# Optimization experiments

Measured on AMD Instinct MI355X. Metric: run time of the kernel, lower is better.

Reference implementation:

```python
import jax, jax.numpy as jnp
import numpy as np

N, D, F = 4096, 4096, 16384  # tokens, d_model, d_ff


def setup_inputs() -> dict:
    key = jax.random.key(0)
    ks = jax.random.split(key, 8)
    q_in = jax.random.randint(ks[0], (N, D), -127, 128, dtype=jnp.int32)
    in_scale = jax.random.uniform(ks[1], (N,), dtype=jnp.float32) * 0.01 + 1e-4
    w1_q = jax.random.randint(ks[2], (F, D), -127, 128, dtype=jnp.int32)
    w1_scale = jax.random.uniform(ks[3], (F,), dtype=jnp.float32) * 0.01 + 1e-4
    b1 = jax.random.normal(ks[4], (F,), dtype=jnp.float32) * 0.02
    w2_q = jax.random.randint(ks[5], (D, F), -127, 128, dtype=jnp.int32)
    w2_scale = jax.random.uniform(ks[6], (D,), dtype=jnp.float32) * 0.01 + 1e-4
    b2 = jax.random.normal(ks[7], (D,), dtype=jnp.float32) * 0.02
    return {"q_in": q_in, "in_scale": in_scale, "w1_q": w1_q, "w1_scale": w1_scale,
            "b1": b1, "w2_q": w2_q, "w2_scale": w2_scale, "b2": b2}


def _dynamic_quant(x):
    # per-token abs-max dynamic quantization to int8 range
    s = jnp.max(jnp.abs(x), axis=-1, keepdims=True) / 127.0
    s = jnp.maximum(s, 1e-8)
    q = jnp.clip(jnp.round(x / s), -128.0, 127.0)
    return q, s


def reference(q_in, in_scale, w1_q, w1_scale, b1, w2_q, w2_scale, b2):
    y1 = jnp.einsum('nd,fd->nf', q_in.astype(jnp.float32), w1_q.astype(jnp.float32))
    y1 = y1 * in_scale[:, None] * w1_scale[None, :] + b1[None, :]
    # fused gelu + dynamic re-quantization epilogue
    a = jax.nn.gelu(y1, approximate=False)
    q2, s2 = _dynamic_quant(a)
    # fc2
    y2 = jnp.einsum('nf,df->nd', q2, w2_q.astype(jnp.float32))
    y2 = y2 * s2 * w2_scale[None, :] + b2[None, :]
    return y2
```

## Files before the change

kernel.cpp:

```cpp
#include <hip/hip_runtime.h>
#include <hip/hip_bf16.h>
#include <cstdint>
#include <math.h>

#define TOKENS 4096
#define DMODEL 4096
#define DFF    16384

typedef __attribute__((ext_vector_type(4))) int i32x4;
typedef __attribute__((address_space(1))) unsigned int glb_u32;
typedef __attribute__((address_space(3))) unsigned int lds_u32;

__global__ void pack_i8_kernel(const int* __restrict__ src, unsigned* __restrict__ dst, long n4) {
    long i = (long)blockIdx.x * blockDim.x + threadIdx.x;
    const long stride = (long)gridDim.x * blockDim.x;
    for (; i < n4; i += stride) {
        const int4 v = ((const int4*)src)[i];
        unsigned p = (unsigned(v.x) & 255u) | ((unsigned(v.y) & 255u) << 8) |
                     ((unsigned(v.z) & 255u) << 16) | ((unsigned(v.w) & 255u) << 24);
        dst[i] = p;
    }
}

__global__ void zero_u32_kernel(unsigned* __restrict__ p, int n) {
    int i = blockIdx.x * blockDim.x + threadIdx.x;
    if (i < n) p[i] = 0u;
}

template <int EPI>
__global__ __launch_bounds__(512)
void gemm_i8_kernel(const int8_t* __restrict__ A,
                    const int8_t* __restrict__ B,
                    const int Nout, const int K,
                    const float* __restrict__ scaleA,
                    const float* __restrict__ scaleB,
                    const float* __restrict__ bias,
                    unsigned* __restrict__ rowmax,
                    __hip_bfloat16* __restrict__ aout,
                    float* __restrict__ out)
{
    __shared__ int8_t As[4][256 * 64];
    __shared__ int8_t Bs[4][256 * 64];

    const int tid  = threadIdx.x;
    const int lane = tid & 63;
    const int w    = tid >> 6;
    const int wm   = w >> 2;
    const int wn   = w & 3;
    const int l15  = lane & 15, l4 = lane >> 4;

    const int gx = gridDim.x, gy = gridDim.y;
    const int wg  = blockIdx.y * gx + blockIdx.x;
    const int xcd = wg & 7;
    const int idx = wg >> 3;
    const int xr = xcd >> 2, xc = xcd & 3;
    const int strip = idx >> 5;
    const int row_t = xr * (gy >> 1) + ((idx & 31) >> 2);
    const int col_t = xc * (gx >> 2) + strip * 4 + (idx & 3);
    const int row0 = row_t * 256;
    const int col0 = col_t * 256;

    const int nt = K >> 6;

    const int g16 = ((lane & 3) ^ ((lane >> 3) & 3)) << 4;

    const int rbA = ((wm << 7) + l15) << 6;
    const int rbB = ((wn << 6) + l15) << 6;
    const int c0  = (l4 ^ ((l15 >> 1) & 3)) << 4;

    i32x4 fA[4], fB[4];
    i32x4 acc[8][4] = {};

#define STAGE_UNIT(P, p0q, LDSARR, bufi, t, u)                                        \
    {                                                                                 \
        const int8_t* src_ = (P) + (size_t)((p0q) + (u) * 128 + (w << 4) +            \
                             (lane >> 2)) * K + ((t) << 6) + g16;                     \
        int8_t* dst_ = &LDSARR[bufi][(u) * 8192 + (w << 10)];                         \
        __builtin_amdgcn_global_load_lds((glb_u32*)src_, (lds_u32*)dst_, 16, 0, 0);   \
    }

#define MFMA_Q(MB)                                                                    \
    {                                                                                 \
        __builtin_amdgcn_s_setprio(1);                                                \
        _Pragma("unroll")                                                             \
        for (int m_ = 0; m_ < 4; ++m_)                                                \
            _Pragma("unroll")                                                         \
            for (int n_ = 0; n_ < 4; ++n_)                                            \
                acc[(MB) + m_][n_] = __builtin_amdgcn_mfma_i32_16x16x64_i8(           \
                    fA[m_], fB[n_], acc[(MB) + m_][n_], 0, 0, 0);                     \
        __builtin_amdgcn_s_setprio(0);                                                \
    }

#pragma unroll
    for (int tt = 0; tt < 3; ++tt) {
        STAGE_UNIT(A, row0, As, tt, tt, 0);
        STAGE_UNIT(A, row0, As, tt, tt, 1);
        STAGE_UNIT(B, col0, Bs, tt, tt, 0);
        STAGE_UNIT(B, col0, Bs, tt, tt, 1);
    }
    asm volatile("s_waitcnt vmcnt(8)" ::: "memory");
    __builtin_amdgcn_s_barrier();

    for (int t = 0; t < nt; ++t) {
        const int buf = t & 3;
        const int tn  = (t + 3 < nt) ? (t + 3) : (nt - 1);
        const int nbuf = tn & 3;

#pragma unroll
        for (int m = 0; m < 4; ++m)
            fA[m] = *(const i32x4*)(&As[buf][rbA + m * 1024 + c0]);
#pragma unroll
        for (int n = 0; n < 4; ++n)
            fB[n] = *(const i32x4*)(&Bs[buf][rbB + n * 1024 + c0]);
        STAGE_UNIT(A, row0, As, nbuf, tn, 0);
        STAGE_UNIT(A, row0, As, nbuf, tn, 1);
        __builtin_amdgcn_sched_barrier(0);
        __builtin_amdgcn_s_barrier();
        asm volatile("s_waitcnt lgkmcnt(0)" ::: "memory");
        __builtin_amdgcn_sched_barrier(0);
        MFMA_Q(0);
        __builtin_amdgcn_s_barrier();

#pragma unroll
        for (int m = 0; m < 4; ++m)
            fA[m] = *(const i32x4*)(&As[buf][rbA + (m + 4) * 1024 + c0]);
        STAGE_UNIT(B, col0, Bs, nbuf, tn, 0);
        STAGE_UNIT(B, col0, Bs, nbuf, tn, 1);
        __builtin_amdgcn_sched_barrier(0);
        __builtin_amdgcn_s_barrier();
        asm volatile("s_waitcnt lgkmcnt(0)" ::: "memory");
        __builtin_amdgcn_sched_barrier(0);
        MFMA_Q(4);
        asm volatile("s_waitcnt vmcnt(8)" ::: "memory");
        __builtin_amdgcn_s_barrier();
    }
#undef STAGE_UNIT
#undef MFMA_Q

    if (EPI == 1) {
#pragma unroll
        for (int m = 0; m < 8; ++m) {
#pragma unroll
            for (int reg = 0; reg < 4; ++reg) {
                const int grow = row0 + (wm << 7) + m * 16 + l4 * 4 + reg;
                const float sa = scaleA[grow];
                float vmax = 0.0f;
#pragma unroll
                for (int n = 0; n < 4; ++n) {
                    const int gcol = col0 + (wn << 6) + n * 16 + l15;
                    const float y = (float)acc[m][n][reg] * sa * scaleB[gcol] + bias[gcol];
                    const float gl = 0.5f * y * (1.0f + erff(y * 0.70710678118654752f));
                    aout[(size_t)grow * DFF + gcol] = __float2bfloat16(gl);
                    vmax = fmaxf(vmax, fabsf(gl));
                }
#pragma unroll
                for (int off = 1; off < 16; off <<= 1)
                    vmax = fmaxf(vmax, __shfl_xor(vmax, off));
                if (l15 == 0) atomicMax(&rowmax[grow], __float_as_uint(vmax));
            }
        }
    } else {
#pragma unroll
        for (int m = 0; m < 8; ++m) {
#pragma unroll
            for (int reg = 0; reg < 4; ++reg) {
                const int grow = row0 + (wm << 7) + m * 16 + l4 * 4 + reg;
                const float s2 = fmaxf(__uint_as_float(rowmax[grow]) * (1.0f / 127.0f), 1e-8f);
#pragma unroll
                for (int n = 0; n < 4; ++n) {
                    const int gcol = col0 + (wn << 6) + n * 16 + l15;
                    out[(size_t)grow * Nout + gcol] =
                        (float)acc[m][n][reg] * s2 * scaleB[gcol] + bias[gcol];
                }
            }
        }
    }
}

__global__ void quant_kernel(const unsigned short* __restrict__ a,
                             const unsigned* __restrict__ rowmax,
                             int8_t* __restrict__ q2)
{
    const size_t nvec = (size_t)TOKENS * DFF / 8;
    size_t i = (size_t)blockIdx.x * blockDim.x + threadIdx.x;
    const size_t stride = (size_t)gridDim.x * blockDim.x;
    for (; i < nvec; i += stride) {
        const size_t e0 = i * 8;
        const int n = (int)(e0 >> 14);
        const float s2 = fmaxf(__uint_as_float(rowmax[n]) * (1.0f / 127.0f), 1e-8f);
        const float inv = 1.0f / s2;
        const uint4 v = *(const uint4*)(a + e0);
        const unsigned words[4] = {v.x, v.y, v.z, v.w};
        int qi[8];
#pragma unroll
        for (int j = 0; j < 4; ++j) {
            const float f0 = __uint_as_float((words[j] & 0xffffu) << 16);
            const float f1 = __uint_as_float(words[j] & 0xffff0000u);
            qi[2 * j]     = (int)fminf(fmaxf(rintf(f0 * inv), -128.0f), 127.0f);
            qi[2 * j + 1] = (int)fminf(fmaxf(rintf(f1 * inv), -128.0f), 127.0f);
        }
        const unsigned p0 = (unsigned(qi[0]) & 255u) | ((unsigned(qi[1]) & 255u) << 8) |
                            ((unsigned(qi[2]) & 255u) << 16) | ((unsigned(qi[3]) & 255u) << 24);
        const unsigned p1 = (unsigned(qi[4]) & 255u) | ((unsigned(qi[5]) & 255u) << 8) |
                            ((unsigned(qi[6]) & 255u) << 16) | ((unsigned(qi[7]) & 255u) << 24);
        ((uint2*)q2)[i] = make_uint2(p0, p1);
    }
}

extern "C" void kernel_launch(void* const* d_in, const int* in_sizes, int n_in,
                              void* d_out, int out_size, void* d_ws, size_t ws_size,
                              hipStream_t stream) {
    const int*   q_in     = (const int*)d_in[0];
    const float* in_scale = (const float*)d_in[1];
    const int*   w1_q     = (const int*)d_in[2];
    const float* w1_scale = (const float*)d_in[3];
    const float* b1       = (const float*)d_in[4];
    const int*   w2_q     = (const int*)d_in[5];
    const float* w2_scale = (const float*)d_in[6];
    const float* b2       = (const float*)d_in[7];
    float* out = (float*)d_out;

    char* ws = (char*)d_ws;
    int8_t* A1 = (int8_t*)(ws);
    int8_t* W1 = (int8_t*)(ws + (size_t)16  * 1048576);
    int8_t* W2 = (int8_t*)(ws + (size_t)80  * 1048576);
    int8_t* Q2 = (int8_t*)(ws + (size_t)144 * 1048576);
    unsigned short* ABUF = (unsigned short*)(ws + (size_t)208 * 1048576);
    unsigned* ROWMAX = (unsigned*)(ws + (size_t)336 * 1048576);

    zero_u32_kernel<<<dim3(16), dim3(256), 0, stream>>>(ROWMAX, TOKENS);
    pack_i8_kernel<<<dim3(1024), dim3(256), 0, stream>>>(q_in, (unsigned*)A1, (long)TOKENS * DMODEL / 4);
    pack_i8_kernel<<<dim3(4096), dim3(256), 0, stream>>>(w1_q, (unsigned*)W1, (long)DFF * DMODEL / 4);
    pack_i8_kernel<<<dim3(4096), dim3(256), 0, stream>>>(w2_q, (unsigned*)W2, (long)DMODEL * DFF / 4);

    gemm_i8_kernel<1><<<dim3(DFF / 256, TOKENS / 256), dim3(512), 0, stream>>>(
        A1, W1, DFF, DMODEL, in_scale, w1_scale, b1, ROWMAX,
        (__hip_bfloat16*)ABUF, nullptr);

    quant_kernel<<<dim3(4096), dim3(256), 0, stream>>>(ABUF, ROWMAX, Q2);

    gemm_i8_kernel<2><<<dim3(DMODEL / 256, TOKENS / 256), dim3(512), 0, stream>>>(
        Q2, W2, DMODEL, DFF, nullptr, w2_scale, b2, ROWMAX,
        nullptr, out);
}
```

Baseline: 978.6 us.

## Use 1024-thread blocks with 16 waves and a 3-stage LDS pipeline

Doubles the GEMM workgroup to 16 waves, so each wave computes a 64x64 sub-tile instead of 128x64. Accumulator registers per wave are halved. The LDS ring shrinks from 4 to 3 stages, and the pipeline is simplified to one global-to-LDS stage per iteration with a single barrier. The interleaved two-half MFMA schedule with sched_barriers is removed. This trades explicit overlap control for more waves to hide latency, at the cost of a shallower prefetch depth and more per-wave fragment-load overhead relative to compute.

After: 904.2 us. 7.6% less time.

```diff
diff --git a/kernel.cpp b/kernel.cpp
--- a/kernel.cpp
+++ b/kernel.cpp
@@ -28,7 +28,7 @@
 }
 
 template <int EPI>
-__global__ __launch_bounds__(512)
+__global__ __launch_bounds__(1024)
 void gemm_i8_kernel(const int8_t* __restrict__ A,
                     const int8_t* __restrict__ B,
                     const int Nout, const int K,
@@ -39,8 +39,8 @@
                     __hip_bfloat16* __restrict__ aout,
                     float* __restrict__ out)
 {
-    __shared__ int8_t As[4][256 * 64];
-    __shared__ int8_t Bs[4][256 * 64];
+    __shared__ int8_t As[3][256 * 64];
+    __shared__ int8_t Bs[3][256 * 64];
 
     const int tid  = threadIdx.x;
     const int lane = tid & 63;
@@ -64,85 +64,67 @@
 
     const int g16 = ((lane & 3) ^ ((lane >> 3) & 3)) << 4;
 
-    const int rbA = ((wm << 7) + l15) << 6;
+    const int rbA = ((wm << 6) + l15) << 6;
     const int rbB = ((wn << 6) + l15) << 6;
     const int c0  = (l4 ^ ((l15 >> 1) & 3)) << 4;
 
-    i32x4 fA[4], fB[4];
-    i32x4 acc[8][4] = {};
-
-#define STAGE_UNIT(P, p0q, LDSARR, bufi, t, u)                                        \
+    i32x4 acc[4][4] = {};
+
+#define STAGE(t, bufi)                                                                \
     {                                                                                 \
-        const int8_t* src_ = (P) + (size_t)((p0q) + (u) * 128 + (w << 4) +            \
-                             (lane >> 2)) * K + ((t) << 6) + g16;                     \
-        int8_t* dst_ = &LDSARR[bufi][(u) * 8192 + (w << 10)];                         \
-        __builtin_amdgcn_global_load_lds((glb_u32*)src_, (lds_u32*)dst_, 16, 0, 0);   \
-    }
-
-#define MFMA_Q(MB)                                                                    \
-    {                                                                                 \
-        __builtin_amdgcn_s_setprio(1);                                                \
-        _Pragma("unroll")                                                             \
-        for (int m_ = 0; m_ < 4; ++m_)                                                \
-            _Pragma("unroll")                                                         \
-            for (int n_ = 0; n_ < 4; ++n_)                                            \
-                acc[(MB) + m_][n_] = __builtin_amdgcn_mfma_i32_16x16x64_i8(           \
-                    fA[m_], fB[n_], acc[(MB) + m_][n_], 0, 0, 0);                     \
-        __builtin_amdgcn_s_setprio(0);                                                \
-    }
-
-#pragma unroll
-    for (int tt = 0; tt < 3; ++tt) {
-        STAGE_UNIT(A, row0, As, tt, tt, 0);
-        STAGE_UNIT(A, row0, As, tt, tt, 1);
-        STAGE_UNIT(B, col0, Bs, tt, tt, 0);
-        STAGE_UNIT(B, col0, Bs, tt, tt, 1);
-    }
-    asm volatile("s_waitcnt vmcnt(8)" ::: "memory");
+        const int8_t* sa_ = A + (size_t)(row0 + (w << 4) + (lane >> 2)) * K +         \
+                            ((t) << 6) + g16;                                         \
+        const int8_t* sb_ = B + (size_t)(col0 + (w << 4) + (lane >> 2)) * K +         \
+                            ((t) << 6) + g16;                                         \
+        __builtin_amdgcn_global_load_lds((glb_u32*)sa_, (lds_u32*)&As[bufi][w << 10], \
+                                         16, 0, 0);                                   \
+        __builtin_amdgcn_global_load_lds((glb_u32*)sb_, (lds_u32*)&Bs[bufi][w << 10], \
+                                         16, 0, 0);                                   \
+    }
+
+    STAGE(0, 0);
+    STAGE(1, 1);
+    asm volatile("s_waitcnt vmcnt(2)" ::: "memory");
     __builtin_amdgcn_s_barrier();
 
+    int buf = 0, sbuf = 2;
     for (int t = 0; t < nt; ++t) {
-        const int buf = t & 3;
-        const int tn  = (t + 3 < nt) ? (t + 3) : (nt - 1);
-        const int nbuf = tn & 3;
-
+        if (t < nt - 2) STAGE(t + 2, sbuf);
+
+        i32x4 fA[4], fB[4];
 #pragma unroll
         for (int m = 0; m < 4; ++m)
             fA[m] = *(const i32x4*)(&As[buf][rbA + m * 1024 + c0]);
 #pragma unroll
         for (int n = 0; n < 4; ++n)
             fB[n] = *(const i32x4*)(&Bs[buf][rbB + n * 1024 + c0]);
-        STAGE_UNIT(A, row0, As, nbuf, tn, 0);
-        STAGE_UNIT(A, row0, As, nbuf, tn, 1);
-        __builtin_amdgcn_sched_barrier(0);
+
+        __builtin_amdgcn_s_setprio(1);
+#pragma unroll
+        for (int m = 0; m < 4; ++m)
+#pragma unroll
+            for (int n = 0; n < 4; ++n)
+                acc[m][n] = __builtin_amdgcn_mfma_i32_16x16x64_i8(fA[m], fB[n], acc[m][n], 0, 0, 0);
+        __builtin_amdgcn_s_setprio(0);
+
+        if (t < nt - 2) {
+            asm volatile("s_waitcnt vmcnt(2)" ::: "memory");
+        } else {
+            asm volatile("s_waitcnt vmcnt(0)" ::: "memory");
+        }
         __builtin_amdgcn_s_barrier();
-        asm volatile("s_waitcnt lgkmcnt(0)" ::: "memory");
-        __builtin_amdgcn_sched_barrier(0);
-        MFMA_Q(0);
-        __builtin_amdgcn_s_barrier();
-
-#pragma unroll
-        for (int m = 0; m < 4; ++m)
-            fA[m] = *(const i32x4*)(&As[buf][rbA + (m + 4) * 1024 + c0]);
-        STAGE_UNIT(B, col0, Bs, nbuf, tn, 0);
-        STAGE_UNIT(B, col0, Bs, nbuf, tn, 1);
-        __builtin_amdgcn_sched_barrier(0);
-        __builtin_amdgcn_s_barrier();
-        asm volatile("s_waitcnt lgkmcnt(0)" ::: "memory");
-        __builtin_amdgcn_sched_barrier(0);
-        MFMA_Q(4);
-        asm volatile("s_waitcnt vmcnt(8)" ::: "memory");
-        __builtin_amdgcn_s_barrier();
-    }
-#undef STAGE_UNIT
-#undef MFMA_Q
+
+        buf  = (buf  == 2) ? 0 : buf + 1;
+        sbuf = (sbuf == 2) ? 0 : sbuf + 1;
+    }
+#undef STAGE
 
     if (EPI == 1) {
 #pragma unroll
-        for (int m = 0; m < 8; ++m) {
+        for (int m = 0; m < 4; ++m) {
 #pragma unroll
             for (int reg = 0; reg < 4; ++reg) {
-                const int grow = row0 + (wm << 7) + m * 16 + l4 * 4 + reg;
+                const int grow = row0 + (wm << 6) + m * 16 + l4 * 4 + reg;
                 const float sa = scaleA[grow];
                 float vmax = 0.0f;
 #pragma unroll
@@ -161,10 +143,10 @@
         }
     } else {
 #pragma unroll
-        for (int m = 0; m < 8; ++m) {
+        for (int m = 0; m < 4; ++m) {
 #pragma unroll
             for (int reg = 0; reg < 4; ++reg) {
-                const int grow = row0 + (wm << 7) + m * 16 + l4 * 4 + reg;
+                const int grow = row0 + (wm << 6) + m * 16 + l4 * 4 + reg;
                 const float s2 = fmaxf(__uint_as_float(rowmax[grow]) * (1.0f / 127.0f), 1e-8f);
 #pragma unroll
                 for (int n = 0; n < 4; ++n) {
@@ -233,13 +215,13 @@
     pack_i8_kernel<<<dim3(4096), dim3(256), 0, stream>>>(w1_q, (unsigned*)W1, (long)DFF * DMODEL / 4);
     pack_i8_kernel<<<dim3(4096), dim3(256), 0, stream>>>(w2_q, (unsigned*)W2, (long)DMODEL * DFF / 4);
 
-    gemm_i8_kernel<1><<<dim3(DFF / 256, TOKENS / 256), dim3(512), 0, stream>>>(
+    gemm_i8_kernel<1><<<dim3(DFF / 256, TOKENS / 256), dim3(1024), 0, stream>>>(
         A1, W1, DFF, DMODEL, in_scale, w1_scale, b1, ROWMAX,
         (__hip_bfloat16*)ABUF, nullptr);
 
     quant_kernel<<<dim3(4096), dim3(256), 0, stream>>>(ABUF, ROWMAX, Q2);
 
-    gemm_i8_kernel<2><<<dim3(DMODEL / 256, TOKENS / 256), dim3(512), 0, stream>>>(
+    gemm_i8_kernel<2><<<dim3(DMODEL / 256, TOKENS / 256), dim3(1024), 0, stream>>>(
         Q2, W2, DMODEL, DFF, nullptr, w2_scale, b2, ROWMAX,
         nullptr, out);
 }
```
